# Optimization experiments

Measured on AMD Instinct MI355X. Metric: run time of the kernel, lower is better.

The kernel has to match this reference:

```python
import jax, jax.numpy as jnp
import numpy as np

AREA_WIDTH = 3


def setup_inputs() -> dict:
    key = jax.random.key(0)
    ks = jax.random.split(key, 8)
    B, C, H, W = 16, 256, 96, 96
    Cq = C // 8
    s = 0.05
    return {
        "x": jax.random.normal(ks[0], (B, C, H, W), jnp.float32),
        "Wq": jax.random.normal(ks[1], (Cq, C), jnp.float32) * s,
        "bq": jax.random.normal(ks[2], (Cq,), jnp.float32) * s,
        "Wk": jax.random.normal(ks[3], (Cq, C), jnp.float32) * s,
        "bk": jax.random.normal(ks[4], (Cq,), jnp.float32) * s,
        "Wv": jax.random.normal(ks[5], (C, C), jnp.float32) * s,
        "bv": jax.random.normal(ks[6], (C,), jnp.float32) * s,
        "gamma": jax.random.normal(ks[7], (1,), jnp.float32) * s,
    }


def _conv1x1(x, W, b):
    # 1x1 conv == channel GEMM: (B,C,H,W) x (O,C) -> (B,O,H,W)
    return jnp.einsum("bchw,oc->bohw", x, W) + b[None, :, None, None]


def reference(x, Wq, bq, Wk, bk, Wv, bv, gamma):
    aw = AREA_WIDTH
    B, C, H, W = x.shape
    q = _conv1x1(x, Wq, bq)  # (B,Cq,H,W)
    k = _conv1x1(x, Wk, bk)
    v = _conv1x1(x, Wv, bv)  # (B,C,H,W)
    Cq = q.shape[1]
    nh, nw = H // aw, W // aw

    # --- horizontal bands: attention along height within each aw-high band, per column w ---
    qh = q.reshape(B, Cq, nh, aw, W)
    kh = k.reshape(B, Cq, nh, aw, W)
    vh = v.reshape(B, C, nh, aw, W)
    # attn[k,j] = softmax_j( sum_c q[c,k] * key[c,j] )
    attn_h = jax.nn.softmax(jnp.einsum("bcnkw,bcnjw->bnwkj", qh, kh), axis=-1)
    # out[c,j] = sum_k v[c,k] * attn[k,j]  (faithful to torch bmm(v, attn))
    out_h = jnp.einsum("bcnkw,bnwkj->bcnjw", vh, attn_h).reshape(B, C, H, W)

    # --- vertical bands: attention along width within each aw-wide band, per row h ---
    qv = q.reshape(B, Cq, H, nw, aw)
    kv = k.reshape(B, Cq, H, nw, aw)
    vv = v.reshape(B, C, H, nw, aw)
    attn_v = jax.nn.softmax(jnp.einsum("bchnk,bchnj->bhnkj", qv, kv), axis=-1)
    out_v = jnp.einsum("bchnk,bhnkj->bchnj", vv, attn_v).reshape(B, C, H, W)

    return gamma * (out_h + out_v) + x
```

## Files before the change

### kernel.cpp

```cpp
#include <hip/hip_runtime.h>
#include <hip/hip_bf16.h>
#include <cstdint>

#define B_ 16
#define C_ 256
#define CQ 32
#define H_ 96
#define W_ 96
#define HW 9216
#define NBAND 32
#define M_ 320

typedef unsigned short u16;
typedef short bf16x8 __attribute__((ext_vector_type(8)));
typedef float f32x4 __attribute__((ext_vector_type(4)));

__device__ inline u16 f2bf(float f) {
    uint32_t u = __float_as_uint(f);
    u += 0x7FFF + ((u >> 16) & 1);
    return (u16)(u >> 16);
}
__device__ inline float bf2f(u16 s) {
    return __uint_as_float(((uint32_t)s) << 16);
}

__device__ inline void gload_lds16(const void* g, void* l) {
    __builtin_amdgcn_global_load_lds(
        (const __attribute__((address_space(1))) uint32_t*)g,
        (__attribute__((address_space(3))) uint32_t*)l, 16, 0, 0);
}

__global__ __launch_bounds__(256) void wpack_kernel(
    const float* __restrict__ Wq, const float* __restrict__ bq,
    const float* __restrict__ Wk, const float* __restrict__ bk,
    const float* __restrict__ Wv, const float* __restrict__ bv,
    u16* __restrict__ Wb, float* __restrict__ biasb)
{
    int m = blockIdx.x;
    int t = threadIdx.x;
    const float* src = (m < 32) ? (Wq + m * 256)
                     : (m < 64) ? (Wk + (m - 32) * 256)
                                : (Wv + (m - 64) * 256);
    Wb[m * 256 + t] = f2bf(src[t]);
    if (t == 0) {
        biasb[m] = (m < 32) ? bq[m] : (m < 64) ? bk[m - 32] : bv[m - 64];
    }
}

__global__ __launch_bounds__(256) void xpose_kernel(const float* __restrict__ x,
                                                    u16* __restrict__ xT) {
    __shared__ float tile[64][65];
    int s0 = blockIdx.x * 64;
    int c0 = blockIdx.y * 64;
    int b  = blockIdx.z;
    int t = threadIdx.x;

    const float* xb = x + ((size_t)b * C_ + c0) * HW + s0;
    {
        int jj = (t & 15) * 4;
        int i0 = t >> 4;
        #pragma unroll
        for (int r = 0; r < 4; ++r) {
            int i = i0 * 4 + r;
            float4 f = *reinterpret_cast<const float4*>(&xb[(size_t)i * HW + jj]);
            tile[i][jj + 0] = f.x;
            tile[i][jj + 1] = f.y;
            tile[i][jj + 2] = f.z;
            tile[i][jj + 3] = f.w;
        }
    }
    __syncthreads();
    u16* xtb = xT + ((size_t)b * HW + s0) * C_ + c0;
    {
        int i2 = (t & 31) * 2;
        int j0 = t >> 5;
        #pragma unroll
        for (int jj = 0; jj < 8; ++jj) {
            int jw = j0 * 8 + jj;
            uint32_t p = (uint32_t)f2bf(tile[i2][jw])
                       | ((uint32_t)f2bf(tile[i2 + 1][jw]) << 16);
            *reinterpret_cast<uint32_t*>(&xtb[(size_t)jw * C_ + i2]) = p;
        }
    }
}

__global__ __launch_bounds__(512, 4) void qkv_gemm_kernel(
    const u16* __restrict__ xT,
    const u16* __restrict__ Wb, const float* __restrict__ biasb,
    u16* __restrict__ qws, u16* __restrict__ kws,
    u16* __restrict__ vws)
{
    __shared__ u16 lA[M_ * 64];
    __shared__ u16 lB[128 * 64];

    int s0 = blockIdx.x * 128;
    int b  = blockIdx.y;
    int t  = threadIdx.x;
    int w  = t >> 6, l = t & 63;
    int lr = l & 15, lg = l >> 4;
    int wm = w >> 2, wn = w & 3;

    f32x4 acc[10][2] = {};

    int rsub = l >> 3;
    int cb   = l & 7;
    const char* gA = (const char*)Wb;
    const char* gB = (const char*)(xT + ((size_t)b * HW + s0) * C_);

    for (int k0 = 0; k0 < 256; k0 += 64) {
        #pragma unroll
        for (int j = 0; j < 5; ++j) {
            int rbase = (w * 5 + j) * 8;
            int r = rbase + rsub;
            const char* src = gA + (size_t)r * 512 + k0 * 2 + ((cb ^ (r & 7)) * 16);
            gload_lds16(src, (char*)lA + rbase * 128);
        }
        #pragma unroll
        for (int j = 0; j < 2; ++j) {
            int rbase = (w * 2 + j) * 8;
            int r = rbase + rsub;
            const char* src = gB + ((size_t)r * C_ + k0) * 2 + ((cb ^ (r & 7)) * 16);
            gload_lds16(src, (char*)lB + rbase * 128);
        }
        __syncthreads();

        #pragma unroll
        for (int ss = 0; ss < 2; ++ss) {
            int csw = (ss * 4 + lg) ^ (lr & 7);
            bf16x8 bfr[2];
            #pragma unroll
            for (int nf = 0; nf < 2; ++nf) {
                int r = wn * 32 + nf * 16 + lr;
                bfr[nf] = *reinterpret_cast<const bf16x8*>((char*)lB + r * 128 + csw * 16);
            }
            #pragma unroll
            for (int mf = 0; mf < 10; ++mf) {
                int r = wm * 160 + mf * 16 + lr;
                bf16x8 af = *reinterpret_cast<const bf16x8*>((char*)lA + r * 128 + csw * 16);
                acc[mf][0] = __builtin_amdgcn_mfma_f32_16x16x32_bf16(af, bfr[0], acc[mf][0], 0, 0, 0);
                acc[mf][1] = __builtin_amdgcn_mfma_f32_16x16x32_bf16(af, bfr[1], acc[mf][1], 0, 0, 0);
            }
        }
        __syncthreads();
    }

    #pragma unroll
    for (int mf = 0; mf < 10; ++mf) {
        #pragma unroll
        for (int r = 0; r < 4; ++r) {
            int mg = wm * 160 + mf * 16 + lg * 4 + r;
            float bias = biasb[mg];
            #pragma unroll
            for (int nf = 0; nf < 2; ++nf) {
                int s = s0 + wn * 32 + nf * 16 + lr;
                float val = acc[mf][nf][r] + bias;
                if (mg < 32) {
                    qws[((size_t)b * CQ + mg) * HW + s] = f2bf(val);
                } else if (mg < 64) {
                    kws[((size_t)b * CQ + (mg - 32)) * HW + s] = f2bf(val);
                } else {
                    vws[((size_t)b * C_ + (mg - 64)) * HW + s] = f2bf(val);
                }
            }
        }
    }
}

__global__ __launch_bounds__(576) void attnw_kernel(
    const u16* __restrict__ qws, const u16* __restrict__ kws,
    float* __restrict__ wbuf)
{
    __shared__ __align__(16) u16 qkl[2 * CQ * 288];
    int n = blockIdx.x;
    int b = blockIdx.y;
    int t = threadIdx.x;

    u16* ql = qkl;
    u16* kl = qkl + CQ * 288;
    float* gw = wbuf + ((size_t)(b * NBAND + n)) * 1728;

    size_t qbase = (size_t)b * CQ * HW + (size_t)n * 288;
    for (int ch = t; ch < 1152; ch += 576) {
        int cq = ch / 36, off = (ch - cq * 36) * 8;
        *reinterpret_cast<uint4*>(&ql[cq * 288 + off]) =
            *reinterpret_cast<const uint4*>(&qws[qbase + (size_t)cq * HW + off]);
        *reinterpret_cast<uint4*>(&kl[cq * 288 + off]) =
            *reinterpret_cast<const uint4*>(&kws[qbase + (size_t)cq * HW + off]);
    }
    __syncthreads();

    int item = t;
    if (item < 288) {
        int w = item % 96, kk = item / 96;
        float l0 = 0.f, l1 = 0.f, l2 = 0.f;
        for (int c = 0; c < CQ; ++c) {
            float qv = bf2f(ql[c * 288 + kk * 96 + w]);
            l0 += qv * bf2f(kl[c * 288 + w]);
            l1 += qv * bf2f(kl[c * 288 + 96 + w]);
            l2 += qv * bf2f(kl[c * 288 + 192 + w]);
        }
        float m = fmaxf(fmaxf(l0, l1), l2);
        float e0 = __expf(l0 - m), e1 = __expf(l1 - m), e2 = __expf(l2 - m);
        float inv = 1.0f / (e0 + e1 + e2);
        gw[(w * 3 + kk) * 3 + 0] = e0 * inv;
        gw[(w * 3 + kk) * 3 + 1] = e1 * inv;
        gw[(w * 3 + kk) * 3 + 2] = e2 * inv;
    } else {
        int it = item - 288;
        int r = it / 96, c2 = it - r * 96;
        int nw = c2 / 3, kk = c2 - nw * 3;
        int base = r * 96 + nw * 3;
        float l0 = 0.f, l1 = 0.f, l2 = 0.f;
        for (int c = 0; c < CQ; ++c) {
            float qv = bf2f(ql[c * 288 + base + kk]);
            l0 += qv * bf2f(kl[c * 288 + base + 0]);
            l1 += qv * bf2f(kl[c * 288 + base + 1]);
            l2 += qv * bf2f(kl[c * 288 + base + 2]);
        }
        float m = fmaxf(fmaxf(l0, l1), l2);
        float e0 = __expf(l0 - m), e1 = __expf(l1 - m), e2 = __expf(l2 - m);
        float inv = 1.0f / (e0 + e1 + e2);
        float* avp = gw + 864 + (r * 32 + nw) * 9 + kk * 3;
        avp[0] = e0 * inv;
        avp[1] = e1 * inv;
        avp[2] = e2 * inv;
    }
}

__global__ __launch_bounds__(256) void apply_kernel(
    const float* __restrict__ x,
    const u16* __restrict__ vws,
    const float* __restrict__ wbuf,
    const float* __restrict__ gamma,
    float* __restrict__ out)
{
    __shared__ float wsh[1728];
    int cc = blockIdx.x;
    int n  = blockIdx.y;
    int b  = blockIdx.z;
    int t  = threadIdx.x;
    float g = gamma[0];

    const float* gw = wbuf + ((size_t)(b * NBAND + n)) * 1728;
    for (int e = t; e < 432; e += 256)
        reinterpret_cast<float4*>(wsh)[e] = reinterpret_cast<const float4*>(gw)[e];
    __syncthreads();

    int lane = t & 63;
    int nw   = lane & 31;
    int half = lane >> 5;
    int wv   = t >> 6;

    float wa[3][3][3], wb[3][3][3];
    #pragma unroll
    for (int jw = 0; jw < 3; ++jw)
        #pragma unroll
        for (int k = 0; k < 3; ++k)
            #pragma unroll
            for (int r = 0; r < 3; ++r)
                wa[jw][k][r] = wsh[(nw * 3 + jw) * 9 + k * 3 + r];
    #pragma unroll
    for (int r = 0; r < 3; ++r)
        #pragma unroll
        for (int k = 0; k < 3; ++k)
            #pragma unroll
            for (int jw = 0; jw < 3; ++jw)
                wb[r][k][jw] = wsh[864 + (r * 32 + nw) * 9 + k * 3 + jw];

    #pragma unroll
    for (int i = 0; i < 8; ++i) {
        int c = cc * 64 + wv * 16 + i * 2 + half;
        size_t base  = ((size_t)b * C_ + c) * HW + (size_t)n * 288 + nw * 3;
        const u16* vp = vws + base;
        float v[3][3], xr[3][3];
        #pragma unroll
        for (int r = 0; r < 3; ++r) {
            #pragma unroll
            for (int jw = 0; jw < 3; ++jw) {
                v[r][jw]  = bf2f(vp[r * 96 + jw]);
                xr[r][jw] = x[base + r * 96 + jw];
            }
        }
        #pragma unroll
        for (int r = 0; r < 3; ++r) {
            #pragma unroll
            for (int jw = 0; jw < 3; ++jw) {
                float oh = v[0][jw] * wa[jw][0][r]
                         + v[1][jw] * wa[jw][1][r]
                         + v[2][jw] * wa[jw][2][r];
                float ov = v[r][0] * wb[r][0][jw]
                         + v[r][1] * wb[r][1][jw]
                         + v[r][2] * wb[r][2][jw];
                out[base + r * 96 + jw] = g * (oh + ov) + xr[r][jw];
            }
        }
    }
}

extern "C" void kernel_launch(void* const* d_in, const int* in_sizes, int n_in,
                              void* d_out, int out_size, void* d_ws, size_t ws_size,
                              hipStream_t stream) {
    const float* x     = (const float*)d_in[0];
    const float* Wq    = (const float*)d_in[1];
    const float* bq    = (const float*)d_in[2];
    const float* Wk    = (const float*)d_in[3];
    const float* bk    = (const float*)d_in[4];
    const float* Wv    = (const float*)d_in[5];
    const float* bv    = (const float*)d_in[6];
    const float* gamma = (const float*)d_in[7];
    float* out = (float*)d_out;

    u16* xT    = (u16*)d_ws;
    u16* qws   = xT + (size_t)B_ * HW * C_;
    u16* kws   = qws + (size_t)B_ * CQ * HW;
    u16* vws   = kws + (size_t)B_ * CQ * HW;
    u16* Wb    = vws + (size_t)B_ * C_ * HW;
    float* biasb = (float*)(Wb + (size_t)M_ * 256);
    float* wbuf = (float*)d_ws;

    wpack_kernel<<<dim3(M_), 256, 0, stream>>>(Wq, bq, Wk, bk, Wv, bv, Wb, biasb);
    xpose_kernel<<<dim3(HW / 64, C_ / 64, B_), 256, 0, stream>>>(x, xT);
    qkv_gemm_kernel<<<dim3(HW / 128, B_), 512, 0, stream>>>(
        xT, Wb, biasb, qws, kws, vws);
    attnw_kernel<<<dim3(NBAND, B_), 576, 0, stream>>>(qws, kws, wbuf);
    apply_kernel<<<dim3(C_ / 64, NBAND, B_), 256, 0, stream>>>(x, vws, wbuf, gamma, out);
}
```

Measured before the change: 379.0 us.

## Double-buffer activation tiles, read weights from global, vectorize transpose stores

The QKV GEMM stops staging the weight matrix in LDS and has each wave read its A fragments straight from global memory (they are likely cache-resident), which frees LDS for a double-buffered activation tile. The next k-slice is prefetched into the other buffer while MFMAs run on the current one, which removes one barrier per step. The transpose kernel now writes 16-byte packed stores of 8 channels instead of 4-byte stores. The cost is that global weight loads sit directly on the MFMA critical path and may stall if they are not served from cache.

```diff
diff --git a/kernel.cpp b/kernel.cpp
--- a/kernel.cpp
+++ b/kernel.cpp
@@ -71,16 +71,17 @@
     }
     __syncthreads();
     u16* xtb = xT + ((size_t)b * HW + s0) * C_ + c0;
-    {
-        int i2 = (t & 31) * 2;
-        int j0 = t >> 5;
-        #pragma unroll
-        for (int jj = 0; jj < 8; ++jj) {
-            int jw = j0 * 8 + jj;
-            uint32_t p = (uint32_t)f2bf(tile[i2][jw])
-                       | ((uint32_t)f2bf(tile[i2 + 1][jw]) << 16);
-            *reinterpret_cast<uint32_t*>(&xtb[(size_t)jw * C_ + i2]) = p;
-        }
+    #pragma unroll
+    for (int q = 0; q < 2; ++q) {
+        int id = q * 256 + t;
+        int s  = id >> 3;
+        int c8 = (id & 7) * 8;
+        uint4 pk;
+        pk.x = (uint32_t)f2bf(tile[c8 + 0][s]) | ((uint32_t)f2bf(tile[c8 + 1][s]) << 16);
+        pk.y = (uint32_t)f2bf(tile[c8 + 2][s]) | ((uint32_t)f2bf(tile[c8 + 3][s]) << 16);
+        pk.z = (uint32_t)f2bf(tile[c8 + 4][s]) | ((uint32_t)f2bf(tile[c8 + 5][s]) << 16);
+        pk.w = (uint32_t)f2bf(tile[c8 + 6][s]) | ((uint32_t)f2bf(tile[c8 + 7][s]) << 16);
+        *reinterpret_cast<uint4*>(&xtb[(size_t)s * C_ + c8]) = pk;
     }
 }
 
@@ -90,8 +91,7 @@
     u16* __restrict__ qws, u16* __restrict__ kws,
     u16* __restrict__ vws)
 {
-    __shared__ u16 lA[M_ * 64];
-    __shared__ u16 lB[128 * 64];
+    __shared__ u16 lB[2][128 * 64];
 
     int s0 = blockIdx.x * 128;
     int b  = blockIdx.y;
@@ -104,26 +104,29 @@
 
     int rsub = l >> 3;
     int cb   = l & 7;
-    const char* gA = (const char*)Wb;
     const char* gB = (const char*)(xT + ((size_t)b * HW + s0) * C_);
-
+    const u16* gA = Wb + (size_t)(wm * 160) * 256;
+
+    #pragma unroll
+    for (int j = 0; j < 2; ++j) {
+        int rbase = (w * 2 + j) * 8;
+        int r = rbase + rsub;
+        const char* src = gB + ((size_t)r * C_) * 2 + ((cb ^ (r & 7)) * 16);
+        gload_lds16(src, (char*)lB[0] + rbase * 128);
+    }
+    __syncthreads();
+
+    int cur = 0;
     for (int k0 = 0; k0 < 256; k0 += 64) {
-        #pragma unroll
-        for (int j = 0; j < 5; ++j) {
-            int rbase = (w * 5 + j) * 8;
-            int r = rbase + rsub;
-            const char* src = gA + (size_t)r * 512 + k0 * 2 + ((cb ^ (r & 7)) * 16);
-            gload_lds16(src, (char*)lA + rbase * 128);
-        }
-        #pragma unroll
-        for (int j = 0; j < 2; ++j) {
-            int rbase = (w * 2 + j) * 8;
-            int r = rbase + rsub;
-            const char* src = gB + ((size_t)r * C_ + k0) * 2 + ((cb ^ (r & 7)) * 16);
-            gload_lds16(src, (char*)lB + rbase * 128);
-        }
-        __syncthreads();
-
+        if (k0 < 192) {
+            #pragma unroll
+            for (int j = 0; j < 2; ++j) {
+                int rbase = (w * 2 + j) * 8;
+                int r = rbase + rsub;
+                const char* src = gB + ((size_t)r * C_ + (k0 + 64)) * 2 + ((cb ^ (r & 7)) * 16);
+                gload_lds16(src, (char*)lB[cur ^ 1] + rbase * 128);
+            }
+        }
         #pragma unroll
         for (int ss = 0; ss < 2; ++ss) {
             int csw = (ss * 4 + lg) ^ (lr & 7);
@@ -131,17 +134,19 @@
             #pragma unroll
             for (int nf = 0; nf < 2; ++nf) {
                 int r = wn * 32 + nf * 16 + lr;
-                bfr[nf] = *reinterpret_cast<const bf16x8*>((char*)lB + r * 128 + csw * 16);
-            }
+                bfr[nf] = *reinterpret_cast<const bf16x8*>((char*)lB[cur] + r * 128 + csw * 16);
+            }
+            int koff = k0 + (ss * 4 + lg) * 8;
             #pragma unroll
             for (int mf = 0; mf < 10; ++mf) {
-                int r = wm * 160 + mf * 16 + lr;
-                bf16x8 af = *reinterpret_cast<const bf16x8*>((char*)lA + r * 128 + csw * 16);
+                bf16x8 af = *reinterpret_cast<const bf16x8*>(
+                    gA + (size_t)(mf * 16 + lr) * 256 + koff);
                 acc[mf][0] = __builtin_amdgcn_mfma_f32_16x16x32_bf16(af, bfr[0], acc[mf][0], 0, 0, 0);
                 acc[mf][1] = __builtin_amdgcn_mfma_f32_16x16x32_bf16(af, bfr[1], acc[mf][1], 0, 0, 0);
             }
         }
         __syncthreads();
+        cur ^= 1;
     }
 
     #pragma unroll
```

After: 539.0 us. 42.2% more time.
